# Kernel tuning notes

Measured on AMD Instinct MI355X. Metric: run time of the kernel, lower is better.

Reference implementation:

```python
import jax, jax.numpy as jnp
import numpy as np


def squash(x, axis=-1):
    sq = jnp.sum(x * x, axis=axis, keepdims=True)
    return (sq / (1.0 + sq)) * (x / (jnp.sqrt(sq) + 1e-8))


def conv2d(x, w, b, stride):
    y = jax.lax.conv_general_dilated(x, w, (stride, stride), 'VALID',
                                     dimension_numbers=('NCHW', 'OIHW', 'NCHW'))
    return y + b[None, :, None, None]


def setup_inputs():
    key = jax.random.key(0)
    ks = jax.random.split(key, 8)
    B = 512
    return {
        'x': jax.random.uniform(ks[0], (B, 1, 28, 28), jnp.float32),
        'conv_w': 0.1 * jax.random.normal(ks[1], (256, 1, 9, 9), jnp.float32),
        'conv_b': jnp.zeros((256,), jnp.float32),
        'pc_w': 0.02 * jax.random.normal(ks[2], (256, 256, 9, 9), jnp.float32),
        'pc_b': jnp.zeros((256,), jnp.float32),
        'W_route': 0.01 * jax.random.normal(ks[3], (10, 1152, 16, 8), jnp.float32),
        'dec_w1': 0.05 * jax.random.normal(ks[4], (512, 160), jnp.float32),
        'dec_b1': jnp.zeros((512,), jnp.float32),
        'dec_w2': 0.05 * jax.random.normal(ks[5], (1024, 512), jnp.float32),
        'dec_b2': jnp.zeros((1024,), jnp.float32),
        'dec_w3': 0.05 * jax.random.normal(ks[6], (784, 1024), jnp.float32),
        'dec_b3': jnp.zeros((784,), jnp.float32),
    }


def capsnet_forward(x, conv_w, conv_b, pc_w, pc_b, W_route,
                    dec_w1, dec_b1, dec_w2, dec_b2, dec_w3, dec_b3,
                    num_routing=3):
    B = x.shape[0]
    # conv1 + relu: [B,1,28,28] -> [B,256,20,20]
    h = jax.nn.relu(conv2d(x, conv_w, conv_b, 1))
    # primary caps conv: [B,256,20,20] -> [B,256,6,6]
    p = conv2d(h, pc_w, pc_b, 2)
    # reshape (C,H,W flattened, grouped by capsule dim 8) -> [B,1152,8], squash
    caps = squash(p.reshape(B, -1, 8))
    # u_hat[b,o,n,d] = sum_i W[o,n,d,i] * caps[b,n,i]  -> [B,10,1152,16]
    u_hat = jnp.einsum('ondi,bni->bond', W_route, caps)
    u_hat_d = jax.lax.stop_gradient(u_hat)
    # dynamic routing
    b_logit = jnp.zeros((B, 10, 1152), u_hat.dtype)
    for _ in range(num_routing - 1):
        c = jax.nn.softmax(b_logit, axis=1)              # over out caps
        s = jnp.einsum('bond,bon->bod', u_hat_d, c)      # [B,10,16]
        v = squash(s)
        b_logit = b_logit + jnp.einsum('bond,bod->bon', u_hat_d, v)
    c = jax.nn.softmax(b_logit, axis=1)
    s = jnp.einsum('bond,bon->bod', u_hat, c)
    v = squash(s)                                        # [B,10,16]
    logits = jnp.linalg.norm(v, axis=-1)                 # [B,10]
    pred = jax.nn.one_hot(jnp.argmax(logits, axis=-1), 10, dtype=v.dtype)
    dec_in = (v * pred[..., None]).reshape(B, -1)        # [B,160]
    h1 = jax.nn.relu(dec_in @ dec_w1.T + dec_b1)
    h2 = jax.nn.relu(h1 @ dec_w2.T + dec_b2)
    reconstruction = jax.nn.sigmoid(h2 @ dec_w3.T + dec_b3)
    return logits, reconstruction


def reference(x, conv_w, conv_b, pc_w, pc_b, W_route,
              dec_w1, dec_b1, dec_w2, dec_b2, dec_w3, dec_b3):
    return capsnet_forward(x, conv_w, conv_b, pc_w, pc_b, W_route,
                           dec_w1, dec_b1, dec_w2, dec_b2, dec_w3, dec_b3)
```

## Files before the change

kernel.cpp:

```cpp
#include <hip/hip_runtime.h>
#include <math.h>


typedef _Float16 f16x8 __attribute__((ext_vector_type(8)));
typedef float f32x4 __attribute__((ext_vector_type(4)));

__global__ __launch_bounds__(256) void k_conv1(const float* __restrict__ x,
        const float* __restrict__ w, const float* __restrict__ bias,
        _Float16* __restrict__ ahi, _Float16* __restrict__ alo) {
    __shared__ __align__(16) float xs[784];
    const int b = blockIdx.x;
    const int t = threadIdx.x;
    for (int i = t; i < 784; i += 256) xs[i] = x[b * 784 + i];
    __syncthreads();

    float wr[81];
#pragma unroll
    for (int i = 0; i < 81; ++i) wr[i] = w[t * 81 + i];
    const float bv = bias[t];

    for (int oy = 0; oy < 20; ++oy) {
        float acc[20];
#pragma unroll
        for (int px = 0; px < 20; ++px) acc[px] = bv;
#pragma unroll
        for (int ky = 0; ky < 9; ++ky) {
            const float* xrow = &xs[(oy + ky) * 28];
            float xr[28];
#pragma unroll
            for (int j = 0; j < 7; ++j) {
                float4 v4 = *(const float4*)(xrow + j * 4);
                xr[j * 4 + 0] = v4.x; xr[j * 4 + 1] = v4.y;
                xr[j * 4 + 2] = v4.z; xr[j * 4 + 3] = v4.w;
            }
#pragma unroll
            for (int kx = 0; kx < 9; ++kx) {
                const float wv = wr[ky * 9 + kx];
#pragma unroll
                for (int px = 0; px < 20; ++px)
                    acc[px] = fmaf(wv, xr[px + kx], acc[px]);
            }
        }
#pragma unroll
        for (int px = 0; px < 20; ++px) {
            const float v16 = fmaxf(acc[px], 0.f) * 16.f;
            const _Float16 hi = (_Float16)v16;
            const _Float16 lo = (_Float16)(v16 - (float)hi);
            const int idx = (b * 400 + oy * 20 + px) * 256 + t;
            ahi[idx] = hi;
            alo[idx] = lo;
        }
    }
}

__global__ __launch_bounds__(256) void k_wcvt(const float* __restrict__ w2,
        _Float16* __restrict__ whi, _Float16* __restrict__ wlo) {
    const int i = blockIdx.x * 256 + threadIdx.x;
    const int n = i / 20736;
    const int r = i - n * 20736;
    const int tap = r >> 8;
    const int ci = r & 255;
    const float v = w2[(n * 256 + ci) * 81 + tap] * 16.f;
    const _Float16 hi = (_Float16)v;
    whi[i] = hi;
    wlo[i] = (_Float16)(v - (float)hi);
}

__global__ __launch_bounds__(256, 3) void k_conv2m(
        const _Float16* __restrict__ ahi, const _Float16* __restrict__ alo,
        const _Float16* __restrict__ whi, const _Float16* __restrict__ wlo,
        const float* __restrict__ bias, float* __restrict__ p) {
    __shared__ __align__(16) _Float16 lds[24576];
    _Float16* sAhi = lds;
    _Float16* sAlo = lds + 4096;
    _Float16* sBhi = lds + 8192;
    _Float16* sBlo = lds + 16384;

    const int t = threadIdx.x;
    const int l = t & 63, w = t >> 6;
    const int m0 = blockIdx.x * 64;
    const int n0 = blockIdx.y * 128;

    const int sr = l >> 3;
    const int oct = ((l & 7) ^ sr) * 8;
    int apix[2];
#pragma unroll
    for (int i = 0; i < 2; ++i) {
        const int r = w * 8 + sr + i * 32;
        const int m = m0 + r;
        const int b = m / 36, pix = m - b * 36;
        const int oy = pix / 6, ox = pix - oy * 6;
        apix[i] = (b * 400 + oy * 40 + ox * 2) * 256 + oct;
    }
    int wbase[4];
#pragma unroll
    for (int i = 0; i < 4; ++i) {
        const int nr = (i * 4 + w) * 8 + sr;
        wbase[i] = (n0 + nr) * 20736 + oct;
    }

    f32x4 acc[2][4];
#pragma unroll
    for (int mf = 0; mf < 2; ++mf)
#pragma unroll
        for (int nf = 0; nf < 4; ++nf) acc[mf][nf] = (f32x4){0.f, 0.f, 0.f, 0.f};

    const int wm = (w >> 1) * 32, wn = (w & 1) * 64;
    const int lm = l & 15, lk = l >> 4;

    f16x8 rAh[2], rAl[2], rBh[4], rBl[4];
    int ky = 0, kx = 0, ci0 = 0, k0 = 0;

#define C2_LOAD() do { \
        const int koff = (ky * 20 + kx) * 256 + ci0; \
        rAh[0] = *(const f16x8*)(ahi + apix[0] + koff); \
        rAl[0] = *(const f16x8*)(alo + apix[0] + koff); \
        rAh[1] = *(const f16x8*)(ahi + apix[1] + koff); \
        rAl[1] = *(const f16x8*)(alo + apix[1] + koff); \
        _Pragma("unroll") \
        for (int i = 0; i < 4; ++i) { \
            rBh[i] = *(const f16x8*)(whi + wbase[i] + k0); \
            rBl[i] = *(const f16x8*)(wlo + wbase[i] + k0); \
        } \
        ci0 += 64; k0 += 64; \
        if (ci0 == 256) { ci0 = 0; ++kx; if (kx == 9) { kx = 0; ++ky; } } \
    } while (0)

    C2_LOAD();

    for (int step = 0; step < 324; ++step) {
        __syncthreads();
#pragma unroll
        for (int i = 0; i < 2; ++i) {
            *(f16x8*)(sAhi + (i * 4 + w) * 512 + l * 8) = rAh[i];
            *(f16x8*)(sAlo + (i * 4 + w) * 512 + l * 8) = rAl[i];
        }
#pragma unroll
        for (int i = 0; i < 4; ++i) {
            *(f16x8*)(sBhi + (i * 4 + w) * 512 + l * 8) = rBh[i];
            *(f16x8*)(sBlo + (i * 4 + w) * 512 + l * 8) = rBl[i];
        }
        __syncthreads();
        if (step < 323) C2_LOAD();

#pragma unroll
        for (int ks = 0; ks < 2; ++ks) {
            const int oj = ks * 4 + lk;
            f16x8 afh[2], afl[2];
#pragma unroll
            for (int mf = 0; mf < 2; ++mf) {
                const int row = wm + mf * 16 + lm;
                const int off = row * 64 + (oj ^ (lm & 7)) * 8;
                afh[mf] = *(const f16x8*)&sAhi[off];
                afl[mf] = *(const f16x8*)&sAlo[off];
            }
#pragma unroll
            for (int nf = 0; nf < 4; ++nf) {
                const int row = wn + nf * 16 + lm;
                const int off = row * 64 + (oj ^ (lm & 7)) * 8;
                const f16x8 bh = *(const f16x8*)&sBhi[off];
                const f16x8 bl = *(const f16x8*)&sBlo[off];
#pragma unroll
                for (int mf = 0; mf < 2; ++mf) {
                    acc[mf][nf] = __builtin_amdgcn_mfma_f32_16x16x32_f16(
                        afh[mf], bh, acc[mf][nf], 0, 0, 0);
                    acc[mf][nf] = __builtin_amdgcn_mfma_f32_16x16x32_f16(
                        afh[mf], bl, acc[mf][nf], 0, 0, 0);
                    acc[mf][nf] = __builtin_amdgcn_mfma_f32_16x16x32_f16(
                        afl[mf], bh, acc[mf][nf], 0, 0, 0);
                }
            }
        }
    }
#undef C2_LOAD

#pragma unroll
    for (int nf = 0; nf < 4; ++nf) {
        const int n = n0 + wn + nf * 16 + lm;
        const float bv = bias[n];
#pragma unroll
        for (int mf = 0; mf < 2; ++mf) {
#pragma unroll
            for (int r = 0; r < 4; ++r) {
                const int m = m0 + wm + mf * 16 + lk * 4 + r;
                const int b = m / 36, pix = m - b * 36;
                p[(b * 256 + n) * 36 + pix] = acc[mf][nf][r] * (1.f / 256.f) + bv;
            }
        }
    }
}

__global__ __launch_bounds__(256) void k_squash(float* __restrict__ pc) {
    const long long i = (long long)blockIdx.x * 256 + threadIdx.x;
    float* p = pc + i * 8;
    float4 v0 = *(float4*)p;
    float4 v1 = *(float4*)(p + 4);
    const float sq = v0.x * v0.x + v0.y * v0.y + v0.z * v0.z + v0.w * v0.w
                   + v1.x * v1.x + v1.y * v1.y + v1.z * v1.z + v1.w * v1.w;
    const float sc = (sq / (1.f + sq)) / (sqrtf(sq) + 1e-8f);
    v0.x *= sc; v0.y *= sc; v0.z *= sc; v0.w *= sc;
    v1.x *= sc; v1.y *= sc; v1.z *= sc; v1.w *= sc;
    *(float4*)p = v0;
    *(float4*)(p + 4) = v1;
}

__global__ __launch_bounds__(128) void k_route(const float* __restrict__ caps,
        const float* __restrict__ W, const float* __restrict__ vsum,
        float* __restrict__ sp, int uniform) {
    const int b = blockIdx.x, nc = blockIdx.y;
    const int t = threadIdx.x;
    const int d = t & 15, g = t >> 4;
    __shared__ float vs[160];
    __shared__ float red[2][160];
    if (uniform == 0)
        for (int i = t; i < 160; i += 128) vs[i] = vsum[b * 160 + i];
    __syncthreads();

    float sacc[10];
#pragma unroll
    for (int o = 0; o < 10; ++o) sacc[o] = 0.f;

    for (int i = 0; i < 16; ++i) {
        const int n = nc * 128 + i * 8 + g;
        const float* cp = caps + ((long long)b * 1152 + n) * 8;
        const float4 ca = *(const float4*)cp;
        const float4 cb = *(const float4*)(cp + 4);
        float uv[10];
#pragma unroll
        for (int o = 0; o < 10; ++o) {
            const float* wp = W + (((long long)o * 1152 + n) * 16 + d) * 8;
            const float4 wa = *(const float4*)wp;
            const float4 wb = *(const float4*)(wp + 4);
            float s = wa.x * ca.x;
            s = fmaf(wa.y, ca.y, s); s = fmaf(wa.z, ca.z, s); s = fmaf(wa.w, ca.w, s);
            s = fmaf(wb.x, cb.x, s); s = fmaf(wb.y, cb.y, s); s = fmaf(wb.z, cb.z, s);
            s = fmaf(wb.w, cb.w, s);
            uv[o] = s;
        }
        float c[10];
        if (uniform) {
#pragma unroll
            for (int o = 0; o < 10; ++o) c[o] = 0.1f;
        } else {
            float dot[10];
#pragma unroll
            for (int o = 0; o < 10; ++o) {
                float xx = uv[o] * vs[o * 16 + d];
                xx += __shfl_xor(xx, 1);
                xx += __shfl_xor(xx, 2);
                xx += __shfl_xor(xx, 4);
                xx += __shfl_xor(xx, 8);
                dot[o] = xx;
            }
            float mx = dot[0];
#pragma unroll
            for (int o = 1; o < 10; ++o) mx = fmaxf(mx, dot[o]);
            float sum = 0.f;
#pragma unroll
            for (int o = 0; o < 10; ++o) { c[o] = expf(dot[o] - mx); sum += c[o]; }
            const float inv = 1.f / sum;
#pragma unroll
            for (int o = 0; o < 10; ++o) c[o] *= inv;
        }
#pragma unroll
        for (int o = 0; o < 10; ++o) sacc[o] = fmaf(c[o], uv[o], sacc[o]);
    }
#pragma unroll
    for (int o = 0; o < 10; ++o) {
        sacc[o] += __shfl_xor(sacc[o], 16);
        sacc[o] += __shfl_xor(sacc[o], 32);
    }
    const int wv = t >> 6;
    if ((t & 63) < 16) {
#pragma unroll
        for (int o = 0; o < 10; ++o) red[wv][o * 16 + d] = sacc[o];
    }
    __syncthreads();
    for (int i = t; i < 160; i += 128)
        sp[((long long)(b * 9 + nc)) * 160 + i] = red[0][i] + red[1][i];
}

__global__ __launch_bounds__(160) void k_squashv(const float* __restrict__ sp,
        float* __restrict__ vsum, float* __restrict__ vbuf, int first) {
    const int b = blockIdx.x, t = threadIdx.x;
    float s = 0.f;
#pragma unroll
    for (int ch = 0; ch < 9; ++ch) s += sp[((long long)(b * 9 + ch)) * 160 + t];
    float sq = s * s;
    sq += __shfl_xor(sq, 1);
    sq += __shfl_xor(sq, 2);
    sq += __shfl_xor(sq, 4);
    sq += __shfl_xor(sq, 8);
    const float sc = (sq / (1.f + sq)) / (sqrtf(sq) + 1e-8f);
    const float v = s * sc;
    vbuf[b * 160 + t] = v;
    vsum[b * 160 + t] = first ? v : (vsum[b * 160 + t] + v);
}

__global__ __launch_bounds__(64) void k_logits(const float* __restrict__ v,
        float* __restrict__ logits, float* __restrict__ dec_in) {
    const int b = blockIdx.x * 64 + threadIdx.x;
    const float* vp = v + (long long)b * 160;
    float nrm[10];
    int amax = 0;
    float best = -1.f;
#pragma unroll
    for (int o = 0; o < 10; ++o) {
        float s = 0.f;
#pragma unroll
        for (int dd = 0; dd < 16; ++dd) { const float xv = vp[o * 16 + dd]; s = fmaf(xv, xv, s); }
        nrm[o] = sqrtf(s);
        if (nrm[o] > best) { best = nrm[o]; amax = o; }
    }
#pragma unroll
    for (int o = 0; o < 10; ++o) logits[b * 10 + o] = nrm[o];
#pragma unroll
    for (int o = 0; o < 10; ++o)
#pragma unroll
        for (int dd = 0; dd < 16; ++dd)
            dec_in[(long long)b * 160 + o * 16 + dd] = (o == amax) ? vp[o * 16 + dd] : 0.f;
}

template <int ACT>
__global__ __launch_bounds__(256) void k_gemm(const float* __restrict__ A,
        const float* __restrict__ W, const float* __restrict__ bias,
        float* __restrict__ C, int N, int K) {
    __shared__ float As[16][68];
    __shared__ float Bs[16][68];
    const int m0 = blockIdx.x * 64, n0 = blockIdx.y * 64;
    const int t = threadIdx.x;
    const int kl = t & 15, rr = t >> 4;
    const int tm = t & 15, tn = t >> 4;

    float acc[4][4];
#pragma unroll
    for (int i = 0; i < 4; ++i)
#pragma unroll
        for (int j = 0; j < 4; ++j) acc[i][j] = 0.f;

    for (int k0 = 0; k0 < K; k0 += 16) {
#pragma unroll
        for (int i = 0; i < 4; ++i) {
            As[kl][rr + i * 16] = A[(m0 + rr + i * 16) * K + k0 + kl];
            const int n = n0 + rr + i * 16;
            Bs[kl][rr + i * 16] = (n < N) ? W[(long long)n * K + k0 + kl] : 0.f;
        }
        __syncthreads();
#pragma unroll
        for (int kk = 0; kk < 16; ++kk) {
            float a[4], bb[4];
#pragma unroll
            for (int i = 0; i < 4; ++i) a[i] = As[kk][tm * 4 + i];
#pragma unroll
            for (int j = 0; j < 4; ++j) bb[j] = Bs[kk][tn * 4 + j];
#pragma unroll
            for (int i = 0; i < 4; ++i)
#pragma unroll
                for (int j = 0; j < 4; ++j)
                    acc[i][j] = fmaf(a[i], bb[j], acc[i][j]);
        }
        __syncthreads();
    }
#pragma unroll
    for (int j = 0; j < 4; ++j) {
        const int n = n0 + tn * 4 + j;
        if (n < N) {
            const float bv = bias[n];
#pragma unroll
            for (int i = 0; i < 4; ++i) {
                const int m = m0 + tm * 4 + i;
                float xv = acc[i][j] + bv;
                if (ACT == 0) xv = fmaxf(xv, 0.f);
                else          xv = 1.f / (1.f + expf(-xv));
                C[(long long)m * N + n] = xv;
            }
        }
    }
}

extern "C" void kernel_launch(void* const* d_in, const int* in_sizes, int n_in,
                              void* d_out, int out_size, void* d_ws, size_t ws_size,
                              hipStream_t stream) {
    const float* x      = (const float*)d_in[0];
    const float* conv_w = (const float*)d_in[1];
    const float* conv_b = (const float*)d_in[2];
    const float* pc_w   = (const float*)d_in[3];
    const float* pc_b   = (const float*)d_in[4];
    const float* Wrt    = (const float*)d_in[5];
    const float* dw1    = (const float*)d_in[6];
    const float* db1    = (const float*)d_in[7];
    const float* dw2    = (const float*)d_in[8];
    const float* db2    = (const float*)d_in[9];
    const float* dw3    = (const float*)d_in[10];
    const float* db3    = (const float*)d_in[11];

    float* out = (float*)d_out;
    char* wsb  = (char*)d_ws;

    _Float16* ahi = (_Float16*)(wsb);
    _Float16* alo = (_Float16*)(wsb + 104857600);
    _Float16* whi = (_Float16*)(wsb + 209715200);
    _Float16* wlo = (_Float16*)(wsb + 220332032);
    float* caps = (float*)(wsb + 230948864);
    float* spart= (float*)(wsb);
    float* vsum = (float*)(wsb + 2949120);
    float* vbuf = (float*)(wsb + 3276800);
    float* din  = (float*)(wsb + 3604480);
    float* h1   = (float*)(wsb + 3932160);
    float* h2   = (float*)(wsb + 4980736);

    k_conv1<<<512, 256, 0, stream>>>(x, conv_w, conv_b, ahi, alo);
    k_wcvt<<<20736, 256, 0, stream>>>(pc_w, whi, wlo);
    k_conv2m<<<dim3(288, 2), 256, 0, stream>>>(ahi, alo, whi, wlo, pc_b, caps);
    k_squash<<<2304, 256, 0, stream>>>(caps);

    k_route<<<dim3(512, 9), 128, 0, stream>>>(caps, Wrt, vsum, spart, 1);
    k_squashv<<<512, 160, 0, stream>>>(spart, vsum, vbuf, 1);
    k_route<<<dim3(512, 9), 128, 0, stream>>>(caps, Wrt, vsum, spart, 0);
    k_squashv<<<512, 160, 0, stream>>>(spart, vsum, vbuf, 0);
    k_route<<<dim3(512, 9), 128, 0, stream>>>(caps, Wrt, vsum, spart, 0);
    k_squashv<<<512, 160, 0, stream>>>(spart, vsum, vbuf, 0);

    k_logits<<<8, 64, 0, stream>>>(vbuf, out, din);

    k_gemm<0><<<dim3(8, 8),  256, 0, stream>>>(din, dw1, db1, h1, 512, 160);
    k_gemm<0><<<dim3(8, 16), 256, 0, stream>>>(h1,  dw2, db2, h2, 1024, 512);
    k_gemm<1><<<dim3(8, 13), 256, 0, stream>>>(h2,  dw3, db3, out + 5120, 784, 1024);
}
```

Baseline: 1.606 ms.

## Enlarge conv2 MFMA tile to 128x128 and split K across two blocks

The primary-caps implicit-GEMM kernel moves from a 64x128 to a 128x128 output tile per block, with each wave computing 64x64. This raises data reuse per LDS load and halves the grid along M. The K reduction is split in two along blockIdx.z, interleaving 64-wide K steps, and partial sums are combined with atomicAdd into an output pre-filled with bias by a new init kernel. The aim is more arithmetic per byte loaded and about the same number of blocks, at the cost of higher register pressure (occupancy bound lowered to 2), float atomics that make the sum order nondeterministic, and an extra init pass.

```diff
diff --git a/kernel.cpp b/kernel.cpp
--- a/kernel.cpp
+++ b/kernel.cpp
@@ -66,102 +66,99 @@
     wlo[i] = (_Float16)(v - (float)hi);
 }
 
-__global__ __launch_bounds__(256, 3) void k_conv2m(
+__global__ __launch_bounds__(256) void k_pinit(const float* __restrict__ bias,
+        float* __restrict__ p) {
+    const int idx = blockIdx.x * 256 + threadIdx.x;
+    const int q = idx / 36;
+    p[idx] = bias[q & 255];
+}
+
+__global__ __launch_bounds__(256, 2) void k_conv2m(
         const _Float16* __restrict__ ahi, const _Float16* __restrict__ alo,
         const _Float16* __restrict__ whi, const _Float16* __restrict__ wlo,
-        const float* __restrict__ bias, float* __restrict__ p) {
-    __shared__ __align__(16) _Float16 lds[24576];
+        float* __restrict__ p) {
+    __shared__ __align__(16) _Float16 lds[32768];
     _Float16* sAhi = lds;
-    _Float16* sAlo = lds + 4096;
-    _Float16* sBhi = lds + 8192;
-    _Float16* sBlo = lds + 16384;
+    _Float16* sAlo = lds + 8192;
+    _Float16* sBhi = lds + 16384;
+    _Float16* sBlo = lds + 24576;
 
     const int t = threadIdx.x;
     const int l = t & 63, w = t >> 6;
-    const int m0 = blockIdx.x * 64;
+    const int m0 = blockIdx.x * 128;
     const int n0 = blockIdx.y * 128;
-
-    const int sr = l >> 3;
-    const int oct = ((l & 7) ^ sr) * 8;
-    int apix[2];
-#pragma unroll
-    for (int i = 0; i < 2; ++i) {
-        const int r = w * 8 + sr + i * 32;
+    const int kz = blockIdx.z;
+
+    const int oct = ((t & 7) ^ ((t >> 3) & 7)) * 8;
+    int apix[4], wbase[4];
+#pragma unroll
+    for (int i = 0; i < 4; ++i) {
+        const int r = i * 32 + (t >> 3);
         const int m = m0 + r;
         const int b = m / 36, pix = m - b * 36;
         const int oy = pix / 6, ox = pix - oy * 6;
         apix[i] = (b * 400 + oy * 40 + ox * 2) * 256 + oct;
-    }
-    int wbase[4];
-#pragma unroll
-    for (int i = 0; i < 4; ++i) {
-        const int nr = (i * 4 + w) * 8 + sr;
-        wbase[i] = (n0 + nr) * 20736 + oct;
-    }
-
-    f32x4 acc[2][4];
-#pragma unroll
-    for (int mf = 0; mf < 2; ++mf)
+        wbase[i] = (n0 + r) * 20736 + oct;
+    }
+
+    f32x4 acc[4][4];
+#pragma unroll
+    for (int mf = 0; mf < 4; ++mf)
 #pragma unroll
         for (int nf = 0; nf < 4; ++nf) acc[mf][nf] = (f32x4){0.f, 0.f, 0.f, 0.f};
 
-    const int wm = (w >> 1) * 32, wn = (w & 1) * 64;
+    const int wm = (w >> 1) * 64, wn = (w & 1) * 64;
     const int lm = l & 15, lk = l >> 4;
 
-    f16x8 rAh[2], rAl[2], rBh[4], rBl[4];
-    int ky = 0, kx = 0, ci0 = 0, k0 = 0;
-
-#define C2_LOAD() do { \
-        const int koff = (ky * 20 + kx) * 256 + ci0; \
-        rAh[0] = *(const f16x8*)(ahi + apix[0] + koff); \
-        rAl[0] = *(const f16x8*)(alo + apix[0] + koff); \
-        rAh[1] = *(const f16x8*)(ahi + apix[1] + koff); \
-        rAl[1] = *(const f16x8*)(alo + apix[1] + koff); \
+    f16x8 rAh[4], rAl[4], rBh[4], rBl[4];
+
+#define C2_LOAD(s) do { \
+        const int tap_ = (s) >> 2; \
+        const int ci0_ = ((s) & 3) << 6; \
+        const int ky_ = tap_ / 9, kx_ = tap_ - ky_ * 9; \
+        const int koff_ = (ky_ * 20 + kx_) * 256 + ci0_; \
+        const int k0_ = (s) * 64; \
         _Pragma("unroll") \
-        for (int i = 0; i < 4; ++i) { \
-            rBh[i] = *(const f16x8*)(whi + wbase[i] + k0); \
-            rBl[i] = *(const f16x8*)(wlo + wbase[i] + k0); \
+        for (int i_ = 0; i_ < 4; ++i_) { \
+            rAh[i_] = *(const f16x8*)(ahi + apix[i_] + koff_); \
+            rAl[i_] = *(const f16x8*)(alo + apix[i_] + koff_); \
+            rBh[i_] = *(const f16x8*)(whi + wbase[i_] + k0_); \
+            rBl[i_] = *(const f16x8*)(wlo + wbase[i_] + k0_); \
         } \
-        ci0 += 64; k0 += 64; \
-        if (ci0 == 256) { ci0 = 0; ++kx; if (kx == 9) { kx = 0; ++ky; } } \
     } while (0)
 
-    C2_LOAD();
-
-    for (int step = 0; step < 324; ++step) {
+    C2_LOAD(kz);
+
+    for (int j = 0; j < 162; ++j) {
         __syncthreads();
 #pragma unroll
-        for (int i = 0; i < 2; ++i) {
-            *(f16x8*)(sAhi + (i * 4 + w) * 512 + l * 8) = rAh[i];
-            *(f16x8*)(sAlo + (i * 4 + w) * 512 + l * 8) = rAl[i];
-        }
-#pragma unroll
         for (int i = 0; i < 4; ++i) {
-            *(f16x8*)(sBhi + (i * 4 + w) * 512 + l * 8) = rBh[i];
-            *(f16x8*)(sBlo + (i * 4 + w) * 512 + l * 8) = rBl[i];
+            *(f16x8*)(sAhi + i * 2048 + t * 8) = rAh[i];
+            *(f16x8*)(sAlo + i * 2048 + t * 8) = rAl[i];
+            *(f16x8*)(sBhi + i * 2048 + t * 8) = rBh[i];
+            *(f16x8*)(sBlo + i * 2048 + t * 8) = rBl[i];
         }
         __syncthreads();
-        if (step < 323) C2_LOAD();
+        if (j < 161) C2_LOAD(2 * (j + 1) + kz);
 
 #pragma unroll
         for (int ks = 0; ks < 2; ++ks) {
-            const int oj = ks * 4 + lk;
-            f16x8 afh[2], afl[2];
-#pragma unroll
-            for (int mf = 0; mf < 2; ++mf) {
+            f16x8 afh[4], afl[4];
+#pragma unroll
+            for (int mf = 0; mf < 4; ++mf) {
                 const int row = wm + mf * 16 + lm;
-                const int off = row * 64 + (oj ^ (lm & 7)) * 8;
+                const int off = row * 64 + ((ks * 4 + lk) ^ (lm & 7)) * 8;
                 afh[mf] = *(const f16x8*)&sAhi[off];
                 afl[mf] = *(const f16x8*)&sAlo[off];
             }
 #pragma unroll
             for (int nf = 0; nf < 4; ++nf) {
                 const int row = wn + nf * 16 + lm;
-                const int off = row * 64 + (oj ^ (lm & 7)) * 8;
+                const int off = row * 64 + ((ks * 4 + lk) ^ (lm & 7)) * 8;
                 const f16x8 bh = *(const f16x8*)&sBhi[off];
                 const f16x8 bl = *(const f16x8*)&sBlo[off];
 #pragma unroll
-                for (int mf = 0; mf < 2; ++mf) {
+                for (int mf = 0; mf < 4; ++mf) {
                     acc[mf][nf] = __builtin_amdgcn_mfma_f32_16x16x32_f16(
                         afh[mf], bh, acc[mf][nf], 0, 0, 0);
                     acc[mf][nf] = __builtin_amdgcn_mfma_f32_16x16x32_f16(
@@ -177,14 +174,14 @@
 #pragma unroll
     for (int nf = 0; nf < 4; ++nf) {
         const int n = n0 + wn + nf * 16 + lm;
-        const float bv = bias[n];
-#pragma unroll
-        for (int mf = 0; mf < 2; ++mf) {
+#pragma unroll
+        for (int mf = 0; mf < 4; ++mf) {
 #pragma unroll
             for (int r = 0; r < 4; ++r) {
                 const int m = m0 + wm + mf * 16 + lk * 4 + r;
                 const int b = m / 36, pix = m - b * 36;
-                p[(b * 256 + n) * 36 + pix] = acc[mf][nf][r] * (1.f / 256.f) + bv;
+                atomicAdd(&p[(b * 256 + n) * 36 + pix],
+                          acc[mf][nf][r] * (1.f / 256.f));
             }
         }
     }
@@ -411,7 +408,8 @@
 
     k_conv1<<<512, 256, 0, stream>>>(x, conv_w, conv_b, ahi, alo);
     k_wcvt<<<20736, 256, 0, stream>>>(pc_w, whi, wlo);
-    k_conv2m<<<dim3(288, 2), 256, 0, stream>>>(ahi, alo, whi, wlo, pc_b, caps);
+    k_pinit<<<18432, 256, 0, stream>>>(pc_b, caps);
+    k_conv2m<<<dim3(144, 2, 2), 256, 0, stream>>>(ahi, alo, whi, wlo, caps);
     k_squash<<<2304, 256, 0, stream>>>(caps);
 
     k_route<<<dim3(512, 9), 128, 0, stream>>>(caps, Wrt, vsum, spart, 1);
```

Result: slower. 1.715 ms (+6.8%).

## Split conv2 reduction four ways with atomics and split conv1 rows across blocks

Applied to the files above, without the earlier changes.

The primary-caps GEMM now splits its K dimension into four interleaved slices across blockIdx.z. It accumulates into an output that a new kernel pre-fills with the bias, using float atomicAdd. This lifts the grid from 576 blocks to 2304 to fill the GPU's CUs better. The load pipeline is also reorganised to double-buffer A registers two steps ahead. Conv1 is split across 5 row groups per image for more parallelism. The costs are atomic traffic, an extra init kernel, and nondeterministic summation order.

```diff
diff --git a/kernel.cpp b/kernel.cpp
--- a/kernel.cpp
+++ b/kernel.cpp
@@ -10,6 +10,7 @@
         _Float16* __restrict__ ahi, _Float16* __restrict__ alo) {
     __shared__ __align__(16) float xs[784];
     const int b = blockIdx.x;
+    const int oy0 = blockIdx.y * 4;
     const int t = threadIdx.x;
     for (int i = t; i < 784; i += 256) xs[i] = x[b * 784 + i];
     __syncthreads();
@@ -19,7 +20,7 @@
     for (int i = 0; i < 81; ++i) wr[i] = w[t * 81 + i];
     const float bv = bias[t];
 
-    for (int oy = 0; oy < 20; ++oy) {
+    for (int oy = oy0; oy < oy0 + 4; ++oy) {
         float acc[20];
 #pragma unroll
         for (int px = 0; px < 20; ++px) acc[px] = bv;
@@ -66,10 +67,17 @@
     wlo[i] = (_Float16)(v - (float)hi);
 }
 
+__global__ __launch_bounds__(256) void k_pinit(const float* __restrict__ bias,
+        float* __restrict__ p) {
+    const int idx = blockIdx.x * 256 + threadIdx.x;
+    const int q = idx / 36;
+    p[idx] = bias[q & 255];
+}
+
 __global__ __launch_bounds__(256, 3) void k_conv2m(
         const _Float16* __restrict__ ahi, const _Float16* __restrict__ alo,
         const _Float16* __restrict__ whi, const _Float16* __restrict__ wlo,
-        const float* __restrict__ bias, float* __restrict__ p) {
+        float* __restrict__ p) {
     __shared__ __align__(16) _Float16 lds[24576];
     _Float16* sAhi = lds;
     _Float16* sAlo = lds + 4096;
@@ -80,6 +88,7 @@
     const int l = t & 63, w = t >> 6;
     const int m0 = blockIdx.x * 64;
     const int n0 = blockIdx.y * 128;
+    const int kz = blockIdx.z;
 
     const int sr = l >> 3;
     const int oct = ((l & 7) ^ sr) * 8;
@@ -108,83 +117,99 @@
     const int wm = (w >> 1) * 32, wn = (w & 1) * 64;
     const int lm = l & 15, lk = l >> 4;
 
-    f16x8 rAh[2], rAl[2], rBh[4], rBl[4];
-    int ky = 0, kx = 0, ci0 = 0, k0 = 0;
-
-#define C2_LOAD() do { \
-        const int koff = (ky * 20 + kx) * 256 + ci0; \
-        rAh[0] = *(const f16x8*)(ahi + apix[0] + koff); \
-        rAl[0] = *(const f16x8*)(alo + apix[0] + koff); \
-        rAh[1] = *(const f16x8*)(ahi + apix[1] + koff); \
-        rAl[1] = *(const f16x8*)(alo + apix[1] + koff); \
+    f16x8 rAh0[2], rAl0[2], rAh1[2], rAl1[2], rBh[4], rBl[4];
+
+#define KOFF(s_) (((((s_) >> 2) / 9) * 20 + (((s_) >> 2) % 9)) * 256 + (((s_) & 3) << 6))
+
+#define LOADA(S, s_) do { \
+        const int koff_ = KOFF(s_); \
+        rAh##S[0] = *(const f16x8*)(ahi + apix[0] + koff_); \
+        rAl##S[0] = *(const f16x8*)(alo + apix[0] + koff_); \
+        rAh##S[1] = *(const f16x8*)(ahi + apix[1] + koff_); \
+        rAl##S[1] = *(const f16x8*)(alo + apix[1] + koff_); \
+    } while (0)
+
+#define LOADB(s_) do { \
+        const int k0_ = (s_) * 64; \
         _Pragma("unroll") \
-        for (int i = 0; i < 4; ++i) { \
-            rBh[i] = *(const f16x8*)(whi + wbase[i] + k0); \
-            rBl[i] = *(const f16x8*)(wlo + wbase[i] + k0); \
+        for (int i_ = 0; i_ < 4; ++i_) { \
+            rBh[i_] = *(const f16x8*)(whi + wbase[i_] + k0_); \
+            rBl[i_] = *(const f16x8*)(wlo + wbase[i_] + k0_); \
         } \
-        ci0 += 64; k0 += 64; \
-        if (ci0 == 256) { ci0 = 0; ++kx; if (kx == 9) { kx = 0; ++ky; } } \
     } while (0)
 
-    C2_LOAD();
-
-    for (int step = 0; step < 324; ++step) {
-        __syncthreads();
-#pragma unroll
-        for (int i = 0; i < 2; ++i) {
-            *(f16x8*)(sAhi + (i * 4 + w) * 512 + l * 8) = rAh[i];
-            *(f16x8*)(sAlo + (i * 4 + w) * 512 + l * 8) = rAl[i];
-        }
-#pragma unroll
-        for (int i = 0; i < 4; ++i) {
-            *(f16x8*)(sBhi + (i * 4 + w) * 512 + l * 8) = rBh[i];
-            *(f16x8*)(sBlo + (i * 4 + w) * 512 + l * 8) = rBl[i];
-        }
-        __syncthreads();
-        if (step < 323) C2_LOAD();
-
-#pragma unroll
-        for (int ks = 0; ks < 2; ++ks) {
-            const int oj = ks * 4 + lk;
-            f16x8 afh[2], afl[2];
-#pragma unroll
-            for (int mf = 0; mf < 2; ++mf) {
-                const int row = wm + mf * 16 + lm;
-                const int off = row * 64 + (oj ^ (lm & 7)) * 8;
-                afh[mf] = *(const f16x8*)&sAhi[off];
-                afl[mf] = *(const f16x8*)&sAlo[off];
-            }
-#pragma unroll
-            for (int nf = 0; nf < 4; ++nf) {
-                const int row = wn + nf * 16 + lm;
-                const int off = row * 64 + (oj ^ (lm & 7)) * 8;
-                const f16x8 bh = *(const f16x8*)&sBhi[off];
-                const f16x8 bl = *(const f16x8*)&sBlo[off];
-#pragma unroll
-                for (int mf = 0; mf < 2; ++mf) {
-                    acc[mf][nf] = __builtin_amdgcn_mfma_f32_16x16x32_f16(
-                        afh[mf], bh, acc[mf][nf], 0, 0, 0);
-                    acc[mf][nf] = __builtin_amdgcn_mfma_f32_16x16x32_f16(
-                        afh[mf], bl, acc[mf][nf], 0, 0, 0);
-                    acc[mf][nf] = __builtin_amdgcn_mfma_f32_16x16x32_f16(
-                        afl[mf], bh, acc[mf][nf], 0, 0, 0);
-                }
-            }
-        }
-    }
-#undef C2_LOAD
+#define MFMA_PHASE() do { \
+        _Pragma("unroll") \
+        for (int ks = 0; ks < 2; ++ks) { \
+            f16x8 afh[2], afl[2]; \
+            _Pragma("unroll") \
+            for (int mf = 0; mf < 2; ++mf) { \
+                const int row = wm + mf * 16 + lm; \
+                const int off = row * 64 + ((ks * 4 + lk) ^ (lm & 7)) * 8; \
+                afh[mf] = *(const f16x8*)&sAhi[off]; \
+                afl[mf] = *(const f16x8*)&sAlo[off]; \
+            } \
+            _Pragma("unroll") \
+            for (int nf = 0; nf < 4; ++nf) { \
+                const int row = wn + nf * 16 + lm; \
+                const int off = row * 64 + ((ks * 4 + lk) ^ (lm & 7)) * 8; \
+                const f16x8 bh = *(const f16x8*)&sBhi[off]; \
+                const f16x8 bl = *(const f16x8*)&sBlo[off]; \
+                _Pragma("unroll") \
+                for (int mf = 0; mf < 2; ++mf) { \
+                    acc[mf][nf] = __builtin_amdgcn_mfma_f32_16x16x32_f16( \
+                        afh[mf], bh, acc[mf][nf], 0, 0, 0); \
+                    acc[mf][nf] = __builtin_amdgcn_mfma_f32_16x16x32_f16( \
+                        afh[mf], bl, acc[mf][nf], 0, 0, 0); \
+                    acc[mf][nf] = __builtin_amdgcn_mfma_f32_16x16x32_f16( \
+                        afl[mf], bh, acc[mf][nf], 0, 0, 0); \
+                } \
+            } \
+        } \
+    } while (0)
+
+#define BODY(jv, S) do { \
+        __syncthreads(); \
+        *(f16x8*)(sAhi + (0 * 4 + w) * 512 + l * 8) = rAh##S[0]; \
+        *(f16x8*)(sAlo + (0 * 4 + w) * 512 + l * 8) = rAl##S[0]; \
+        *(f16x8*)(sAhi + (1 * 4 + w) * 512 + l * 8) = rAh##S[1]; \
+        *(f16x8*)(sAlo + (1 * 4 + w) * 512 + l * 8) = rAl##S[1]; \
+        _Pragma("unroll") \
+        for (int i_ = 0; i_ < 4; ++i_) { \
+            *(f16x8*)(sBhi + (i_ * 4 + w) * 512 + l * 8) = rBh[i_]; \
+            *(f16x8*)(sBlo + (i_ * 4 + w) * 512 + l * 8) = rBl[i_]; \
+        } \
+        __syncthreads(); \
+        if ((jv) + 2 <= 80) LOADA(S, 4 * ((jv) + 2) + kz); \
+        if ((jv) + 1 <= 80) LOADB(4 * ((jv) + 1) + kz); \
+        MFMA_PHASE(); \
+    } while (0)
+
+    LOADA(0, kz);
+    LOADA(1, 4 + kz);
+    LOADB(kz);
+
+    for (int jj = 0; jj < 41; ++jj) {
+        BODY(2 * jj, 0);
+        if (jj < 40) BODY(2 * jj + 1, 1);
+    }
+#undef BODY
+#undef MFMA_PHASE
+#undef LOADB
+#undef LOADA
+#undef KOFF
 
 #pragma unroll
     for (int nf = 0; nf < 4; ++nf) {
         const int n = n0 + wn + nf * 16 + lm;
-        const float bv = bias[n];
 #pragma unroll
         for (int mf = 0; mf < 2; ++mf) {
 #pragma unroll
             for (int r = 0; r < 4; ++r) {
                 const int m = m0 + wm + mf * 16 + lk * 4 + r;
                 const int b = m / 36, pix = m - b * 36;
-                p[(b * 256 + n) * 36 + pix] = acc[mf][nf][r] * (1.f / 256.f) + bv;
+                atomicAdd(&p[(b * 256 + n) * 36 + pix],
+                          acc[mf][nf][r] * (1.f / 256.f));
             }
         }
     }
@@ -409,9 +434,10 @@
     float* h1   = (float*)(wsb + 3932160);
     float* h2   = (float*)(wsb + 4980736);
 
-    k_conv1<<<512, 256, 0, stream>>>(x, conv_w, conv_b, ahi, alo);
+    k_conv1<<<dim3(512, 5), 256, 0, stream>>>(x, conv_w, conv_b, ahi, alo);
     k_wcvt<<<20736, 256, 0, stream>>>(pc_w, whi, wlo);
-    k_conv2m<<<dim3(288, 2), 256, 0, stream>>>(ahi, alo, whi, wlo, pc_b, caps);
+    k_pinit<<<18432, 256, 0, stream>>>(pc_b, caps);
+    k_conv2m<<<dim3(288, 2, 4), 256, 0, stream>>>(ahi, alo, whi, wlo, caps);
     k_squash<<<2304, 256, 0, stream>>>(caps);
 
     k_route<<<dim3(512, 9), 128, 0, stream>>>(caps, Wrt, vsum, spart, 1);
```

New measurement: 1.708 ms. 1.06x slower.
